# Performance work log

Hardware: AMD Instinct MI355X
Metric: run time of the kernel (lower is better)

Reference implementation:

```python
import jax, jax.numpy as jnp
import numpy as np
from jax import lax

DN = ('NHWC', 'HWIO', 'NHWC')
EPS = 1e-7


def squash(s, axis=-1):
    sq = jnp.sum(s * s, axis=axis, keepdims=True)
    return s * (sq / (1.0 + sq) / jnp.sqrt(sq + EPS))


def setup_inputs() -> dict:
    key = jax.random.key(0)
    ks = jax.random.split(key, 4)
    inputs = jax.random.normal(ks[0], (2, 250, 250, 3), dtype=jnp.float32)
    conv_w = jax.random.normal(ks[1], (9, 9, 3, 256), dtype=jnp.float32) * 0.02
    conv_b = jnp.zeros((256,), dtype=jnp.float32)
    pc_w = jax.random.normal(ks[2], (9, 9, 256, 128), dtype=jnp.float32) * 0.02
    pc_b = jnp.zeros((128,), dtype=jnp.float32)
    # CapsLayer routing weights: [num_caps=8, in_caps=219024, dim_caps=8, in_dim=8]
    W_caps = jax.random.normal(ks[3], (8, 219024, 8, 8), dtype=jnp.float32) * 0.05
    return {"inputs": inputs, "conv_w": conv_w, "conv_b": conv_b,
            "pc_w": pc_w, "pc_b": pc_b, "W_caps": W_caps}


def reference(inputs, conv_w, conv_b, pc_w, pc_b, W_caps):
    ROUTINGS = 3
    B = inputs.shape[0]
    # Conv backbone: 250x250x3 -> 242x242x256, ReLU
    x = lax.conv_general_dilated(inputs, conv_w, (1, 1), 'VALID', dimension_numbers=DN)
    x = jax.nn.relu(x + conv_b)
    # PrimaryCaps: linear conv (128 ch, k=9, s=2, valid) -> 117x117x128 -> [B, 219024, 8] -> squash
    pc = lax.conv_general_dilated(x, pc_w, (2, 2), 'VALID', dimension_numbers=DN) + pc_b
    u = squash(pc.reshape(B, -1, 8))  # [B, N=219024, 8]
    # Prediction vectors u_hat[b,j,i,o] = W[j,i,o,d] u[b,i,d]
    u_hat = jnp.einsum('jiod,bid->bjio', W_caps, u)  # [B, J, N, 8]
    J, N = W_caps.shape[0], W_caps.shape[1]
    b_logits = jnp.zeros((B, J, N), dtype=u_hat.dtype)
    v = None
    for r in range(ROUTINGS):
        c = jax.nn.softmax(b_logits, axis=1)          # coupling over output caps
        s = jnp.einsum('bji,bjio->bjo', c, u_hat)     # [B, J, 8]
        v = squash(s)
        if r < ROUTINGS - 1:
            b_logits = b_logits + jnp.einsum('bjo,bjio->bji', v, u_hat)
    return v  # [B, 8, 8]
```

## Files before the change

### kernel.cpp

```cpp
#include <hip/hip_runtime.h>

#define N_CAPS 219024
#define J_CAPS 8

typedef __attribute__((ext_vector_type(8))) __bf16 bf16x8;
typedef __attribute__((ext_vector_type(4))) float  f32x4;
typedef __attribute__((ext_vector_type(8))) short  short8;

__device__ __forceinline__ unsigned short f2bf(float f) {
    unsigned int u = __float_as_uint(f);
    u = (u + 0x7FFFu + ((u >> 16) & 1u)) >> 16;
    return (unsigned short)u;
}

__global__ __launch_bounds__(256) void conv1_kernel(
    const float* __restrict__ in, const float* __restrict__ w,
    const float* __restrict__ bias, unsigned short* __restrict__ out)
{
    const int oc  = threadIdx.x;
    const int ox0 = blockIdx.x * 16;
    const int oy  = blockIdx.y;
    const int b   = blockIdx.z;

    __shared__ float lin[9][24][3];
    for (int idx = threadIdx.x; idx < 9 * 24 * 3; idx += 256) {
        int r   = idx / (24 * 3);
        int rem = idx - r * (24 * 3);
        int col = rem / 3;
        int c   = rem - col * 3;
        int iy  = oy + r;
        int ix  = ox0 + col;
        float v = 0.f;
        if (ix < 250) v = in[((b * 250 + iy) * 250 + ix) * 3 + c];
        lin[r][col][c] = v;
    }
    __syncthreads();

    float acc[16];
#pragma unroll
    for (int t = 0; t < 16; ++t) acc[t] = 0.f;

    for (int ky = 0; ky < 9; ++ky) {
#pragma unroll
        for (int ic = 0; ic < 3; ++ic) {
            float xv[24];
#pragma unroll
            for (int c2 = 0; c2 < 24; ++c2) xv[c2] = lin[ky][c2][ic];
#pragma unroll
            for (int kx = 0; kx < 9; ++kx) {
                float wv = w[((ky * 9 + kx) * 3 + ic) * 256 + oc];
#pragma unroll
                for (int t = 0; t < 16; ++t)
                    acc[t] += xv[kx + t] * wv;
            }
        }
    }

    float bv = bias[oc];
#pragma unroll
    for (int t = 0; t < 16; ++t) {
        int ox = ox0 + t;
        if (ox < 242) {
            float v = acc[t] + bv;
            out[((b * 242 + oy) * 242 + ox) * 256 + oc] = f2bf(v > 0.f ? v : 0.f);
        }
    }
}

__global__ __launch_bounds__(256) void w2_convert_kernel(
    const float* __restrict__ w, unsigned short* __restrict__ wt)
{
    int idx = blockIdx.x * 256 + threadIdx.x;
    if (idx >= 81 * 128 * 256) return;
    int ic = idx & 255;
    int t  = idx >> 8;
    int oc = t & 127;
    int p  = t >> 7;
    wt[idx] = f2bf(w[(p * 256 + ic) * 128 + oc]);
}

__global__ __launch_bounds__(256) void conv2_mfma_kernel(
    const unsigned short* __restrict__ x1bf,
    const unsigned short* __restrict__ w2t,
    const float* __restrict__ bias,
    float* __restrict__ out)
{
    const int bx   = blockIdx.x;
    const int oy   = blockIdx.y;
    const int b    = blockIdx.z;
    const int tid  = threadIdx.x;
    const int wave = tid >> 6;
    const int lane = tid & 63;
    const int li   = lane & 15;
    const int quad = lane >> 4;
    const int wm   = (wave & 1) * 32;
    const int wn   = (wave >> 1) * 64;
    const int ox0  = bx * 64;

    __shared__ __align__(16) unsigned short As[135 * 64];
    __shared__ __align__(16) unsigned short Bs[128 * 64];

    f32x4 acc[2][4];
#pragma unroll
    for (int mt = 0; mt < 2; ++mt)
#pragma unroll
        for (int nt = 0; nt < 4; ++nt)
            acc[mt][nt] = (f32x4){0.f, 0.f, 0.f, 0.f};

    for (int ky = 0; ky < 9; ++ky) {
        const int iy = 2 * oy + ky;
        const unsigned short* xrow = x1bf + ((size_t)(b * 242 + iy) * 242) * 256;
        for (int hq = 0; hq < 4; ++hq) {
            __syncthreads();
            for (int idx = tid; idx < 135 * 8; idx += 256) {
                int c    = idx >> 3;
                int kkc  = idx & 7;
                int gcol = 2 * ox0 + c;
                short8 v = {0, 0, 0, 0, 0, 0, 0, 0};
                if (gcol < 242)
                    v = *(const short8*)&xrow[(size_t)gcol * 256 + hq * 64 + kkc * 8];
                *(short8*)&As[c * 64 + ((kkc ^ ((c >> 1) & 7)) * 8)] = v;
            }
            for (int kx = 0; kx < 9; ++kx) {
                __syncthreads();
                const unsigned short* wp = w2t + (size_t)(ky * 9 + kx) * 128 * 256;
                for (int idx = tid; idx < 128 * 8; idx += 256) {
                    int n   = idx >> 3;
                    int kkc = idx & 7;
                    *(short8*)&Bs[n * 64 + ((kkc ^ (n & 7)) * 8)] =
                        *(const short8*)&wp[(size_t)n * 256 + hq * 64 + kkc * 8];
                }
                __syncthreads();
#pragma unroll
                for (int kh = 0; kh < 2; ++kh) {
                    const int ch = kh * 4 + quad;
                    const int c0 = 2 * (wm + li) + kx;
                    const int c1 = 2 * (wm + 16 + li) + kx;
                    bf16x8 a0 = *(const bf16x8*)&As[c0 * 64 + ((ch ^ ((c0 >> 1) & 7)) * 8)];
                    bf16x8 a1 = *(const bf16x8*)&As[c1 * 64 + ((ch ^ ((c1 >> 1) & 7)) * 8)];
                    const int n0 = wn + li;
                    const int n1 = wn + 16 + li;
                    const int n2 = wn + 32 + li;
                    const int n3 = wn + 48 + li;
                    bf16x8 b0 = *(const bf16x8*)&Bs[n0 * 64 + ((ch ^ (n0 & 7)) * 8)];
                    bf16x8 b1 = *(const bf16x8*)&Bs[n1 * 64 + ((ch ^ (n1 & 7)) * 8)];
                    bf16x8 b2 = *(const bf16x8*)&Bs[n2 * 64 + ((ch ^ (n2 & 7)) * 8)];
                    bf16x8 b3 = *(const bf16x8*)&Bs[n3 * 64 + ((ch ^ (n3 & 7)) * 8)];
                    acc[0][0] = __builtin_amdgcn_mfma_f32_16x16x32_bf16(a0, b0, acc[0][0], 0, 0, 0);
                    acc[0][1] = __builtin_amdgcn_mfma_f32_16x16x32_bf16(a0, b1, acc[0][1], 0, 0, 0);
                    acc[0][2] = __builtin_amdgcn_mfma_f32_16x16x32_bf16(a0, b2, acc[0][2], 0, 0, 0);
                    acc[0][3] = __builtin_amdgcn_mfma_f32_16x16x32_bf16(a0, b3, acc[0][3], 0, 0, 0);
                    acc[1][0] = __builtin_amdgcn_mfma_f32_16x16x32_bf16(a1, b0, acc[1][0], 0, 0, 0);
                    acc[1][1] = __builtin_amdgcn_mfma_f32_16x16x32_bf16(a1, b1, acc[1][1], 0, 0, 0);
                    acc[1][2] = __builtin_amdgcn_mfma_f32_16x16x32_bf16(a1, b2, acc[1][2], 0, 0, 0);
                    acc[1][3] = __builtin_amdgcn_mfma_f32_16x16x32_bf16(a1, b3, acc[1][3], 0, 0, 0);
                }
            }
        }
    }

#pragma unroll
    for (int mt = 0; mt < 2; ++mt) {
#pragma unroll
        for (int nt = 0; nt < 4; ++nt) {
            const int oc = wn + nt * 16 + li;
            const float bv = bias[oc];
#pragma unroll
            for (int r = 0; r < 4; ++r) {
                const int m  = wm + mt * 16 + quad * 4 + r;
                const int ox = ox0 + m;
                if (ox < 117)
                    out[((size_t)(b * 117 + oy) * 117 + ox) * 128 + oc] = acc[mt][nt][r] + bv;
            }
        }
    }
}

__global__ __launch_bounds__(256) void squash_u_kernel(float* data, int n_groups)
{
    int i = blockIdx.x * 256 + threadIdx.x;
    if (i >= n_groups) return;
    float4* p = (float4*)(data + (size_t)i * 8);
    float4 a = p[0], c = p[1];
    float sq = a.x * a.x + a.y * a.y + a.z * a.z + a.w * a.w
             + c.x * c.x + c.y * c.y + c.z * c.z + c.w * c.w;
    float scale = (sq / (1.f + sq)) * rsqrtf(sq + 1e-7f);
    p[0] = make_float4(a.x * scale, a.y * scale, a.z * scale, a.w * scale);
    p[1] = make_float4(c.x * scale, c.y * scale, c.z * scale, c.w * scale);
}

__global__ __launch_bounds__(256) void uhat_kernel(
    const float* __restrict__ W, const float* __restrict__ u,
    float* __restrict__ uhat)
{
    int idx = blockIdx.x * 256 + threadIdx.x;
    if (idx >= J_CAPS * N_CAPS) return;
    int j = idx / N_CAPS;
    int i = idx - j * N_CAPS;

    const float4* wp = (const float4*)(W + (size_t)idx * 64);
    const float4* u0 = (const float4*)(u + (size_t)i * 8);
    const float4* u1 = (const float4*)(u + ((size_t)N_CAPS + i) * 8);
    float4 u0a = u0[0], u0b = u0[1];
    float4 u1a = u1[0], u1b = u1[1];

    float o0[8], o1[8];
#pragma unroll
    for (int o = 0; o < 8; ++o) {
        float4 wa = wp[2 * o], wb = wp[2 * o + 1];
        o0[o] = wa.x * u0a.x + wa.y * u0a.y + wa.z * u0a.z + wa.w * u0a.w
              + wb.x * u0b.x + wb.y * u0b.y + wb.z * u0b.z + wb.w * u0b.w;
        o1[o] = wa.x * u1a.x + wa.y * u1a.y + wa.z * u1a.z + wa.w * u1a.w
              + wb.x * u1b.x + wb.y * u1b.y + wb.z * u1b.z + wb.w * u1b.w;
    }
    float4* d0 = (float4*)(uhat + ((size_t)(0 * J_CAPS + j) * N_CAPS + i) * 8);
    float4* d1 = (float4*)(uhat + ((size_t)(1 * J_CAPS + j) * N_CAPS + i) * 8);
    d0[0] = make_float4(o0[0], o0[1], o0[2], o0[3]);
    d0[1] = make_float4(o0[4], o0[5], o0[6], o0[7]);
    d1[0] = make_float4(o1[0], o1[1], o1[2], o1[3]);
    d1[1] = make_float4(o1[4], o1[5], o1[6], o1[7]);
}

template <int MODE>
__global__ __launch_bounds__(256) void routing_kernel(
    const float* __restrict__ uhat, const float* __restrict__ vprev,
    const float* __restrict__ b_in, float* __restrict__ b_out,
    float* __restrict__ s)
{
    const int bb = blockIdx.y;
    __shared__ float vsh[64];
    __shared__ float ssh[64];
    if (threadIdx.x < 64) {
        ssh[threadIdx.x] = 0.f;
        vsh[threadIdx.x] = (MODE > 0) ? vprev[bb * 64 + threadIdx.x] : 0.f;
    }
    __syncthreads();

    float acc[64];
#pragma unroll
    for (int k = 0; k < 64; ++k) acc[k] = 0.f;

    const float* ub = uhat + (size_t)bb * J_CAPS * (size_t)N_CAPS * 8;
    for (int i = blockIdx.x * 256 + threadIdx.x; i < N_CAPS; i += gridDim.x * 256) {
        float uh[64];
#pragma unroll
        for (int j = 0; j < 8; ++j) {
            const float* p = ub + ((size_t)j * N_CAPS + i) * 8;
            float4 x0 = *(const float4*)p;
            float4 x1 = *(const float4*)(p + 4);
            uh[j * 8 + 0] = x0.x; uh[j * 8 + 1] = x0.y;
            uh[j * 8 + 2] = x0.z; uh[j * 8 + 3] = x0.w;
            uh[j * 8 + 4] = x1.x; uh[j * 8 + 5] = x1.y;
            uh[j * 8 + 6] = x1.z; uh[j * 8 + 7] = x1.w;
        }
        float c[8];
        if (MODE == 0) {
#pragma unroll
            for (int j = 0; j < 8; ++j) c[j] = 0.125f;
        } else {
            float bj[8];
#pragma unroll
            for (int j = 0; j < 8; ++j) {
                float d = 0.f;
#pragma unroll
                for (int o = 0; o < 8; ++o) d += vsh[j * 8 + o] * uh[j * 8 + o];
                bj[j] = d;
            }
            if (MODE == 2) {
#pragma unroll
                for (int j = 0; j < 8; ++j)
                    bj[j] += b_in[((size_t)bb * 8 + j) * N_CAPS + i];
            } else {
#pragma unroll
                for (int j = 0; j < 8; ++j)
                    b_out[((size_t)bb * 8 + j) * N_CAPS + i] = bj[j];
            }
            float m = bj[0];
#pragma unroll
            for (int j = 1; j < 8; ++j) m = fmaxf(m, bj[j]);
            float se = 0.f;
#pragma unroll
            for (int j = 0; j < 8; ++j) { c[j] = __expf(bj[j] - m); se += c[j]; }
            float inv = 1.f / se;
#pragma unroll
            for (int j = 0; j < 8; ++j) c[j] *= inv;
        }
#pragma unroll
        for (int k = 0; k < 64; ++k) acc[k] += c[k >> 3] * uh[k];
    }

#pragma unroll
    for (int k = 0; k < 64; ++k) {
        float v = acc[k];
        for (int off = 32; off > 0; off >>= 1)
            v += __shfl_down(v, off, 64);
        if ((threadIdx.x & 63) == 0) atomicAdd(&ssh[k], v);
    }
    __syncthreads();
    if (threadIdx.x < 64) atomicAdd(&s[bb * 64 + threadIdx.x], ssh[threadIdx.x]);
}

__global__ void squash_v_kernel(const float* __restrict__ s, float* __restrict__ v)
{
    int t = threadIdx.x;
    if (t >= 16) return;
    const float4* p = (const float4*)(s + t * 8);
    float4 a = p[0], c = p[1];
    float sq = a.x * a.x + a.y * a.y + a.z * a.z + a.w * a.w
             + c.x * c.x + c.y * c.y + c.z * c.z + c.w * c.w;
    float scale = (sq / (1.f + sq)) * rsqrtf(sq + 1e-7f);
    float4* d = (float4*)(v + t * 8);
    d[0] = make_float4(a.x * scale, a.y * scale, a.z * scale, a.w * scale);
    d[1] = make_float4(c.x * scale, c.y * scale, c.z * scale, c.w * scale);
}

__global__ void zero_kernel(float* p, int n)
{
    int i = blockIdx.x * 256 + threadIdx.x;
    if (i < n) p[i] = 0.f;
}

extern "C" void kernel_launch(void* const* d_in, const int* in_sizes, int n_in,
                              void* d_out, int out_size, void* d_ws, size_t ws_size,
                              hipStream_t stream)
{
    const float* in = (const float*)d_in[0];
    const float* w1 = (const float*)d_in[1];
    const float* b1 = (const float*)d_in[2];
    const float* w2 = (const float*)d_in[3];
    const float* b2 = (const float*)d_in[4];
    const float* Wc = (const float*)d_in[5];
    float* out = (float*)d_out;
    char* wsb  = (char*)d_ws;

    float*          uhat = (float*)wsb;
    unsigned short* x1bf = (unsigned short*)wsb;
    float*          pc   = (float*)(wsb + 112140288);
    float*          blog = (float*)(wsb + 126157824);
    unsigned short* w2t  = (unsigned short*)(wsb + 140175360);
    float*          sbuf = (float*)(wsb + 145483776);
    float*          vbuf = (float*)(wsb + 145484288);

    w2_convert_kernel<<<(81 * 128 * 256 + 255) / 256, 256, 0, stream>>>(w2, w2t);
    conv1_kernel<<<dim3(16, 242, 2), 256, 0, stream>>>(in, w1, b1, x1bf);
    conv2_mfma_kernel<<<dim3(2, 117, 2), 256, 0, stream>>>(x1bf, w2t, b2, pc);
    squash_u_kernel<<<(2 * N_CAPS + 255) / 256, 256, 0, stream>>>(pc, 2 * N_CAPS);
    uhat_kernel<<<(J_CAPS * N_CAPS + 255) / 256, 256, 0, stream>>>(Wc, pc, uhat);

    zero_kernel<<<1, 128, 0, stream>>>(sbuf, 128);
    routing_kernel<0><<<dim3(256, 2), 256, 0, stream>>>(uhat, nullptr, nullptr, nullptr, sbuf);
    squash_v_kernel<<<1, 64, 0, stream>>>(sbuf, vbuf);

    zero_kernel<<<1, 128, 0, stream>>>(sbuf, 128);
    routing_kernel<1><<<dim3(256, 2), 256, 0, stream>>>(uhat, vbuf, nullptr, blog, sbuf);
    squash_v_kernel<<<1, 64, 0, stream>>>(sbuf, vbuf);

    zero_kernel<<<1, 128, 0, stream>>>(sbuf, 128);
    routing_kernel<2><<<dim3(256, 2), 256, 0, stream>>>(uhat, vbuf, blog, nullptr, sbuf);
    squash_v_kernel<<<1, 64, 0, stream>>>(sbuf, out);
}
```

Measured before the change: 1.516 ms.

## Stream conv2 weights from global and stage 128-channel activation tiles

Restructures the strided conv2 MFMA kernel. Weight fragments are now loaded straight from global memory into registers instead of through LDS. Activations are staged in 128-channel chunks, which removes the per-kx barriers and B-tile copies. Waves now split only across output channels, and each wave computes all 64 output columns. The activation loader also drops the zero-fill bounds check, so it may read past the end of the buffer for the last row, and it relies on cache hits for the repeated global weight loads.

```diff
diff --git a/kernel.cpp b/kernel.cpp
--- a/kernel.cpp
+++ b/kernel.cpp
@@ -93,84 +93,78 @@
     const int lane = tid & 63;
     const int li   = lane & 15;
     const int quad = lane >> 4;
-    const int wm   = (wave & 1) * 32;
-    const int wn   = (wave >> 1) * 64;
+    const int wn   = wave * 32;
     const int ox0  = bx * 64;
 
-    __shared__ __align__(16) unsigned short As[135 * 64];
-    __shared__ __align__(16) unsigned short Bs[128 * 64];
-
-    f32x4 acc[2][4];
-#pragma unroll
-    for (int mt = 0; mt < 2; ++mt)
-#pragma unroll
-        for (int nt = 0; nt < 4; ++nt)
-            acc[mt][nt] = (f32x4){0.f, 0.f, 0.f, 0.f};
+    __shared__ __align__(16) unsigned short As[135 * 128];
+
+    f32x4 acc[4][2];
+#pragma unroll
+    for (int mt = 0; mt < 4; ++mt) {
+        acc[mt][0] = (f32x4){0.f, 0.f, 0.f, 0.f};
+        acc[mt][1] = (f32x4){0.f, 0.f, 0.f, 0.f};
+    }
+
+    const int n0 = wn + li;
+    const int n1 = wn + 16 + li;
+    const size_t bofs0 = (size_t)n0 * 256 + quad * 8;
+    const size_t bofs1 = (size_t)n1 * 256 + quad * 8;
 
     for (int ky = 0; ky < 9; ++ky) {
         const int iy = 2 * oy + ky;
-        const unsigned short* xrow = x1bf + ((size_t)(b * 242 + iy) * 242) * 256;
-        for (int hq = 0; hq < 4; ++hq) {
+        const unsigned short* xrow =
+            x1bf + ((size_t)(b * 242 + iy) * 242 + 2 * ox0) * 256;
+
+        for (int hq = 0; hq < 2; ++hq) {
             __syncthreads();
-            for (int idx = tid; idx < 135 * 8; idx += 256) {
-                int c    = idx >> 3;
-                int kkc  = idx & 7;
-                int gcol = 2 * ox0 + c;
-                short8 v = {0, 0, 0, 0, 0, 0, 0, 0};
-                if (gcol < 242)
-                    v = *(const short8*)&xrow[(size_t)gcol * 256 + hq * 64 + kkc * 8];
-                *(short8*)&As[c * 64 + ((kkc ^ ((c >> 1) & 7)) * 8)] = v;
-            }
+            for (int it = 0; it < 9; ++it) {
+                int ct = it * 256 + tid;
+                if (ct < 135 * 16) {
+                    int col = ct >> 4;
+                    int cc  = ct & 15;
+                    int src = cc ^ ((col >> 1) & 7);
+                    *(short8*)&As[ct * 8] =
+                        *(const short8*)&xrow[col * 256 + hq * 128 + src * 8];
+                }
+            }
+            __syncthreads();
+
+            const size_t bo0 = bofs0 + hq * 128;
+            const size_t bo1 = bofs1 + hq * 128;
+
             for (int kx = 0; kx < 9; ++kx) {
-                __syncthreads();
-                const unsigned short* wp = w2t + (size_t)(ky * 9 + kx) * 128 * 256;
-                for (int idx = tid; idx < 128 * 8; idx += 256) {
-                    int n   = idx >> 3;
-                    int kkc = idx & 7;
-                    *(short8*)&Bs[n * 64 + ((kkc ^ (n & 7)) * 8)] =
-                        *(const short8*)&wp[(size_t)n * 256 + hq * 64 + kkc * 8];
+                const unsigned short* wp = w2t + ((size_t)(ky * 9 + kx) << 15);
+                const int colbase = (li << 1) + kx;
+                const int sw = (li + (kx >> 1)) & 7;
+                const unsigned short* abase = As + colbase * 128;
+#pragma unroll
+                for (int kc = 0; kc < 4; ++kc) {
+                    bf16x8 b0 = *(const bf16x8*)&wp[bo0 + kc * 32];
+                    bf16x8 b1 = *(const bf16x8*)&wp[bo1 + kc * 32];
+                    const int chs = ((kc << 2) + quad) ^ sw;
+#pragma unroll
+                    for (int mt = 0; mt < 4; ++mt) {
+                        bf16x8 a = *(const bf16x8*)&abase[mt * 4096 + chs * 8];
+                        acc[mt][0] = __builtin_amdgcn_mfma_f32_16x16x32_bf16(a, b0, acc[mt][0], 0, 0, 0);
+                        acc[mt][1] = __builtin_amdgcn_mfma_f32_16x16x32_bf16(a, b1, acc[mt][1], 0, 0, 0);
+                    }
                 }
-                __syncthreads();
-#pragma unroll
-                for (int kh = 0; kh < 2; ++kh) {
-                    const int ch = kh * 4 + quad;
-                    const int c0 = 2 * (wm + li) + kx;
-                    const int c1 = 2 * (wm + 16 + li) + kx;
-                    bf16x8 a0 = *(const bf16x8*)&As[c0 * 64 + ((ch ^ ((c0 >> 1) & 7)) * 8)];
-                    bf16x8 a1 = *(const bf16x8*)&As[c1 * 64 + ((ch ^ ((c1 >> 1) & 7)) * 8)];
-                    const int n0 = wn + li;
-                    const int n1 = wn + 16 + li;
-                    const int n2 = wn + 32 + li;
-                    const int n3 = wn + 48 + li;
-                    bf16x8 b0 = *(const bf16x8*)&Bs[n0 * 64 + ((ch ^ (n0 & 7)) * 8)];
-                    bf16x8 b1 = *(const bf16x8*)&Bs[n1 * 64 + ((ch ^ (n1 & 7)) * 8)];
-                    bf16x8 b2 = *(const bf16x8*)&Bs[n2 * 64 + ((ch ^ (n2 & 7)) * 8)];
-                    bf16x8 b3 = *(const bf16x8*)&Bs[n3 * 64 + ((ch ^ (n3 & 7)) * 8)];
-                    acc[0][0] = __builtin_amdgcn_mfma_f32_16x16x32_bf16(a0, b0, acc[0][0], 0, 0, 0);
-                    acc[0][1] = __builtin_amdgcn_mfma_f32_16x16x32_bf16(a0, b1, acc[0][1], 0, 0, 0);
-                    acc[0][2] = __builtin_amdgcn_mfma_f32_16x16x32_bf16(a0, b2, acc[0][2], 0, 0, 0);
-                    acc[0][3] = __builtin_amdgcn_mfma_f32_16x16x32_bf16(a0, b3, acc[0][3], 0, 0, 0);
-                    acc[1][0] = __builtin_amdgcn_mfma_f32_16x16x32_bf16(a1, b0, acc[1][0], 0, 0, 0);
-                    acc[1][1] = __builtin_amdgcn_mfma_f32_16x16x32_bf16(a1, b1, acc[1][1], 0, 0, 0);
-                    acc[1][2] = __builtin_amdgcn_mfma_f32_16x16x32_bf16(a1, b2, acc[1][2], 0, 0, 0);
-                    acc[1][3] = __builtin_amdgcn_mfma_f32_16x16x32_bf16(a1, b3, acc[1][3], 0, 0, 0);
-                }
-            }
-        }
-    }
-
-#pragma unroll
-    for (int mt = 0; mt < 2; ++mt) {
-#pragma unroll
-        for (int nt = 0; nt < 4; ++nt) {
-            const int oc = wn + nt * 16 + li;
-            const float bv = bias[oc];
-#pragma unroll
-            for (int r = 0; r < 4; ++r) {
-                const int m  = wm + mt * 16 + quad * 4 + r;
-                const int ox = ox0 + m;
-                if (ox < 117)
-                    out[((size_t)(b * 117 + oy) * 117 + ox) * 128 + oc] = acc[mt][nt][r] + bv;
+            }
+        }
+    }
+
+    const float bv0 = bias[n0];
+    const float bv1 = bias[n1];
+#pragma unroll
+    for (int mt = 0; mt < 4; ++mt) {
+#pragma unroll
+        for (int r = 0; r < 4; ++r) {
+            const int m  = mt * 16 + quad * 4 + r;
+            const int ox = ox0 + m;
+            if (ox < 117) {
+                float* op = &out[((size_t)(b * 117 + oy) * 117 + ox) * 128];
+                op[n0] = acc[mt][0][r] + bv0;
+                op[n1] = acc[mt][1][r] + bv1;
             }
         }
     }
```

Result: faster. 1.313 ms (-13.4%).
